# Optimization experiments

Hardware: AMD Instinct MI355X
Metric: run time of the kernel (lower is better)

The kernel has to match this reference:

```python
import jax, jax.numpy as jnp
import numpy as np

EPS = 1e-8

def _layernorm(x, gamma, beta):
    # torch-style: std with Bessel correction (ddof=1), eps added to std
    D = x.shape[-1]
    mean = jnp.mean(x, axis=-1, keepdims=True)
    var = jnp.sum((x - mean) ** 2, axis=-1, keepdims=True) / (D - 1)
    std = jnp.sqrt(var)
    return (x - mean) / (std + EPS) * gamma + beta


def setup_inputs() -> dict:
    key = jax.random.key(0)
    B, T, D, H = 1, 2048, 1024, 16
    Dh = D // H
    ks = jax.random.split(key, 8)
    s = 0.02
    return {
        "x": jax.random.normal(ks[0], (B, T, D), jnp.float32),
        "wq": jax.random.normal(ks[1], (H, D, Dh), jnp.float32) * s,
        "wk": jax.random.normal(ks[2], (H, D, Dh), jnp.float32) * s,
        "wv": jax.random.normal(ks[3], (H, D, Dh), jnp.float32) * s,
        "wo": jax.random.normal(ks[4], (D, D), jnp.float32) * s,
        "bo": jnp.zeros((D,), jnp.float32),
        "ln1_g": jnp.ones((D,), jnp.float32),
        "ln1_b": jnp.zeros((D,), jnp.float32),
        "ln2_g": jnp.ones((D,), jnp.float32),
        "ln2_b": jnp.zeros((D,), jnp.float32),
        "w1": jax.random.normal(ks[5], (D, 4 * D), jnp.float32) * s,
        "b1": jnp.zeros((4 * D,), jnp.float32),
        "w2": jax.random.normal(ks[6], (4 * D, D), jnp.float32) * s,
        "b2": jnp.zeros((D,), jnp.float32),
    }


def reference(x, wq, wk, wv, wo, bo, ln1_g, ln1_b, ln2_g, ln2_b, w1, b1, w2, b2):
    B, T, D = x.shape
    H, _, Dh = wq.shape
    # --- attention sublayer (dropout p used at eval => identity) ---
    h = _layernorm(x, ln1_g, ln1_b)
    q = jnp.einsum('btd,hde->bhte', h, wq)
    k = jnp.einsum('btd,hde->bhte', h, wk)
    v = jnp.einsum('btd,hde->bhte', h, wv)
    scores = jnp.einsum('bhte,bhse->bhts', q, k) / jnp.sqrt(jnp.float32(Dh))
    causal = jnp.triu(jnp.ones((T, T), bool), 1)  # True above diagonal => masked
    scores = jnp.where(causal, -jnp.inf, scores)
    attn = jax.nn.softmax(scores, axis=-1)
    ctx = jnp.einsum('bhts,bhse->bthe', attn, v).reshape(B, T, H * Dh)
    att_out = ctx @ wo + bo
    x = x + att_out
    # --- FFN sublayer ---
    h2 = _layernorm(x, ln2_g, ln2_b)
    ffn = jax.nn.gelu(h2 @ w1 + b1, approximate=False) @ w2 + b2
    return x + ffn
```

## Files before the change

kernel.cpp:

```cpp
#include <hip/hip_runtime.h>
#include <hip/hip_bf16.h>
#include <math.h>

typedef unsigned short bf16u;
typedef __attribute__((ext_vector_type(8))) short short8;
typedef __attribute__((ext_vector_type(4))) float floatx4;

__device__ __forceinline__ float bf2f(bf16u u) {
  union { unsigned int i; float f; } c;
  c.i = ((unsigned int)u) << 16;
  return c.f;
}
__device__ __forceinline__ bf16u f2bf(float f) {
  union { float f; unsigned int i; } c;
  c.f = f;
  unsigned int lsb = (c.i >> 16) & 1u;
  c.i += 0x7fffu + lsb;
  return (bf16u)(c.i >> 16);
}

__device__ __forceinline__ void load_lds16(const void* g, void* l) {
  __builtin_amdgcn_global_load_lds(
      (const __attribute__((address_space(1))) void*)g,
      (__attribute__((address_space(3))) void*)l, 16, 0, 0);
}

__global__ __launch_bounds__(256) void ln_kernel(
    const float* __restrict__ x, bf16u* __restrict__ out,
    const float* __restrict__ gamma, const float* __restrict__ beta) {
  const int row = blockIdx.x;
  const int tid = threadIdx.x;
  const int lane = tid & 63, wave = tid >> 6;
  __shared__ float red[4];
  const float* xr = x + (size_t)row * 1024;
  float v[4];
#pragma unroll
  for (int i = 0; i < 4; i++) v[i] = xr[tid + i * 256];
  float s = v[0] + v[1] + v[2] + v[3];
#pragma unroll
  for (int off = 32; off; off >>= 1) s += __shfl_down(s, off);
  if (lane == 0) red[wave] = s;
  __syncthreads();
  const float mean = (red[0] + red[1] + red[2] + red[3]) * (1.0f / 1024.0f);
  __syncthreads();
  float sq = 0.f;
#pragma unroll
  for (int i = 0; i < 4; i++) { float d = v[i] - mean; sq += d * d; }
#pragma unroll
  for (int off = 32; off; off >>= 1) sq += __shfl_down(sq, off);
  if (lane == 0) red[wave] = sq;
  __syncthreads();
  const float var = (red[0] + red[1] + red[2] + red[3]) * (1.0f / 1023.0f);
  const float inv = 1.0f / (sqrtf(var) + 1e-8f);
  bf16u* orow = out + (size_t)row * 1024;
#pragma unroll
  for (int i = 0; i < 4; i++) {
    int idx = tid + i * 256;
    orow[idx] = f2bf((v[i] - mean) * inv * gamma[idx] + beta[idx]);
  }
}

__global__ __launch_bounds__(256) void pack_weights(
    const float* __restrict__ wq, const float* __restrict__ wk,
    const float* __restrict__ wv, const float* __restrict__ wo,
    const float* __restrict__ w1, const float* __restrict__ w2,
    bf16u* __restrict__ WqkvT, bf16u* __restrict__ woT,
    bf16u* __restrict__ w1T, bf16u* __restrict__ w2T) {
  __shared__ bf16u tile[32][33];
  const int id = blockIdx.x;
  const float* in; bf16u* out; int R, C, bx, by;
  if (id < 3072) {
    int job = id >> 10, rem = id & 1023;
    int head = rem >> 6, t = rem & 63;
    bx = t & 1; by = t >> 1;
    in = (job == 0 ? wq : (job == 1 ? wk : wv)) + head * 65536;
    out = WqkvT + job * 1048576 + head * 65536;
    R = 1024; C = 64;
  } else if (id < 4096) {
    int rem = id - 3072; bx = rem & 31; by = rem >> 5;
    in = wo; out = woT; R = 1024; C = 1024;
  } else if (id < 8192) {
    int rem = id - 4096; bx = rem & 127; by = rem >> 7;
    in = w1; out = w1T; R = 1024; C = 4096;
  } else {
    int rem = id - 8192; bx = rem & 31; by = rem >> 5;
    in = w2; out = w2T; R = 4096; C = 1024;
  }
  const int bc = bx * 32, br = by * 32;
  const int lx = threadIdx.x & 31, ly = threadIdx.x >> 5;
#pragma unroll
  for (int i = 0; i < 32; i += 8)
    tile[ly + i][lx] = f2bf(in[(size_t)(br + ly + i) * C + bc + lx]);
  __syncthreads();
#pragma unroll
  for (int i = 0; i < 32; i += 8)
    out[(size_t)(bc + ly + i) * R + br + lx] = tile[lx][ly + i];
}

__global__ __launch_bounds__(256) void transpose_b(
    const bf16u* __restrict__ in, bf16u* __restrict__ out,
    int ins, int coff, int outs) {
  __shared__ bf16u tile[32][33];
  const int bc = blockIdx.x * 32, br = blockIdx.y * 32;
  const int lx = threadIdx.x & 31, ly = threadIdx.x >> 5;
#pragma unroll
  for (int i = 0; i < 32; i += 8)
    tile[ly + i][lx] = in[(size_t)(br + ly + i) * ins + coff + bc + lx];
  __syncthreads();
#pragma unroll
  for (int i = 0; i < 32; i += 8)
    out[(size_t)(bc + ly + i) * outs + br + lx] = tile[lx][ly + i];
}

template <int BM, int BN, int WGR, int WGC, int EPI>
__global__ __launch_bounds__(256, 4) void gemm_bt(
    const bf16u* __restrict__ A, const bf16u* __restrict__ Bt,
    const float* __restrict__ bias, const float* __restrict__ res,
    void* __restrict__ Cout, int M, int N, int K, int kchunk) {
  constexpr int BK = 64;
  constexpr int TM = BM / WGR, TN = BN / WGC;
  constexpr int NI = TM / 16, NJ = TN / 16;
  alignas(16) __shared__ bf16u sA[BM * BK];
  alignas(16) __shared__ bf16u sB[BN * BK];
  const int tid = threadIdx.x, lane = tid & 63, wave = tid >> 6;
  const int wr = wave / WGC, wc = wave % WGC;
  const int quad = lane >> 4, l16 = lane & 15;
  const int m0 = blockIdx.y * BM, n0 = blockIdx.x * BN;
  const int kz = blockIdx.z;
  const int kbeg = kz * kchunk;
  const int kend = (kbeg + kchunk < K) ? (kbeg + kchunk) : K;

  floatx4 acc[NI][NJ] = {};
  constexpr int ACH = BM * BK / 8;
  constexpr int BCH = BN * BK / 8;

  for (int k0 = kbeg; k0 < kend; k0 += BK) {
#pragma unroll
    for (int c = tid; c < ACH; c += 256) {
      int r = c >> 3, kc = ((c ^ r) & 7) * 8;
      load_lds16(A + (size_t)(m0 + r) * K + k0 + kc, (void*)(sA + c * 8));
    }
#pragma unroll
    for (int c = tid; c < BCH; c += 256) {
      int r = c >> 3, kc = ((c ^ r) & 7) * 8;
      load_lds16(Bt + (size_t)(n0 + r) * K + k0 + kc, (void*)(sB + c * 8));
    }
    __syncthreads();
#pragma unroll
    for (int kk = 0; kk < BK; kk += 32) {
      const int ch = (kk >> 3) + quad;
      short8 af[NI], bf[NJ];
#pragma unroll
      for (int i = 0; i < NI; i++) {
        const int R = wr * TM + i * 16 + l16;
        af[i] = *(const short8*)(sA + R * BK + ((ch ^ (R & 7)) << 3));
      }
#pragma unroll
      for (int j = 0; j < NJ; j++) {
        const int R = wc * TN + j * 16 + l16;
        bf[j] = *(const short8*)(sB + R * BK + ((ch ^ (R & 7)) << 3));
      }
#pragma unroll
      for (int i = 0; i < NI; i++)
#pragma unroll
        for (int j = 0; j < NJ; j++)
          acc[i][j] = __builtin_amdgcn_mfma_f32_16x16x32_bf16(af[i], bf[j], acc[i][j], 0, 0, 0);
    }
    __syncthreads();
  }

  float* pout = (float*)Cout;
  if constexpr (EPI == 3) pout += (size_t)kz * M * N;
#pragma unroll
  for (int j = 0; j < NJ; j++) {
    const int col = n0 + wc * TN + j * 16 + l16;
    float bv = 0.0f;
    if constexpr (EPI == 1 || EPI == 2) bv = bias[col];
#pragma unroll
    for (int i = 0; i < NI; i++) {
#pragma unroll
      for (int r = 0; r < 4; r++) {
        const int row = m0 + wr * TM + i * 16 + quad * 4 + r;
        const size_t o = (size_t)row * N + col;
        const float v = acc[i][j][r];
        if constexpr (EPI == 0) {
          ((bf16u*)Cout)[o] = f2bf(v);
        } else if constexpr (EPI == 1) {
          pout[o] = v + bv + res[o];
        } else if constexpr (EPI == 2) {
          float t = v + bv;
          ((bf16u*)Cout)[o] = f2bf(0.5f * t * (1.0f + erff(t * 0.70710678118654752f)));
        } else {
          pout[o] = v;
        }
      }
    }
  }
}

__global__ __launch_bounds__(256) void reduce2_kernel(
    const float* __restrict__ part, const float* __restrict__ bias,
    const float* __restrict__ res, float* __restrict__ out,
    int N, size_t total) {
  size_t i = ((size_t)blockIdx.x * 256 + threadIdx.x) * 4;
  if (i >= total) return;
  float4 a = *(const float4*)(part + i);
  float4 b = *(const float4*)(part + total + i);
  float4 r = *(const float4*)(res + i);
  float4 bv = *(const float4*)(bias + (int)(i & (size_t)(N - 1)));
  float4 o;
  o.x = a.x + b.x + r.x + bv.x;
  o.y = a.y + b.y + r.y + bv.y;
  o.z = a.z + b.z + r.z + bv.z;
  o.w = a.w + b.w + r.w + bv.w;
  *(float4*)(out + i) = o;
}

template <int NT, bool MASK>
__device__ __forceinline__ void attn_tile(
    const bf16u* sQ, const bf16u* sK, const bf16u* sVt, bf16u* sP,
    floatx4* aco, floatx4& acc_l, short8 ones,
    int q0, int c0, int wave, int quad, int l16) {
  const int rq = wave * 16 + l16;
  floatx4 s[NT] = {};
#pragma unroll
  for (int kk = 0; kk < 64; kk += 32) {
    const int ch = (kk >> 3) + quad;
    short8 aq = *(const short8*)(sQ + rq * 64 + ((ch ^ (rq & 7)) << 3));
#pragma unroll
    for (int nt = 0; nt < NT; nt++) {
      const int rk = nt * 16 + l16;
      short8 bk = *(const short8*)(sK + rk * 64 + ((ch ^ (rk & 7)) << 3));
      s[nt] = __builtin_amdgcn_mfma_f32_16x16x32_bf16(bk, aq, s[nt], 0, 0, 0);
    }
  }
  const float C = 0.125f * 1.44269504088896f;
  const int qrow = q0 + rq;
#pragma unroll
  for (int nt = 0; nt < NT; nt++)
#pragma unroll
    for (int r = 0; r < 4; r++) {
      float t = s[nt][r] * C;
      if constexpr (MASK) {
        const int kpos = c0 + nt * 16 + quad * 4 + r;
        if (kpos > qrow) t = -__builtin_inff();
      }
      s[nt][r] = __builtin_amdgcn_exp2f(t);
    }
  __syncthreads();
#pragma unroll
  for (int nt = 0; nt < NT; nt++) {
    unsigned int lo = (unsigned int)f2bf(s[nt][0]) | ((unsigned int)f2bf(s[nt][1]) << 16);
    unsigned int hi = (unsigned int)f2bf(s[nt][2]) | ((unsigned int)f2bf(s[nt][3]) << 16);
    uint2 pk; pk.x = lo; pk.y = hi;
    const int e0 = nt * 16 + quad * 4;
    const int cch = e0 >> 3, sub = e0 & 7;
    *(uint2*)(sP + rq * 128 + ((cch ^ (rq & 7)) << 3) + sub) = pk;
  }
  __syncthreads();
#pragma unroll
  for (int kk = 0; kk < NT * 16; kk += 32) {
    const int ch = (kk >> 3) + quad;
    short8 ap = *(const short8*)(sP + rq * 128 + ((ch ^ (rq & 7)) << 3));
#pragma unroll
    for (int dt = 0; dt < 4; dt++) {
      const int rv = dt * 16 + l16;
      short8 bv = *(const short8*)(sVt + rv * 128 + ((ch ^ (rv & 7)) << 3));
      aco[dt] = __builtin_amdgcn_mfma_f32_16x16x32_bf16(ap, bv, aco[dt], 0, 0, 0);
    }
    acc_l = __builtin_amdgcn_mfma_f32_16x16x32_bf16(ap, ones, acc_l, 0, 0, 0);
  }
}

template <int NZ>
__global__ __launch_bounds__(256, 4) void flash_attn(
    const bf16u* __restrict__ QKV, const bf16u* __restrict__ Vt,
    bf16u* __restrict__ partO, float* __restrict__ partL) {
  const int qb = 31 - blockIdx.x;
  const int h = blockIdx.y;
  const int z = blockIdx.z;
  const int tid = threadIdx.x, lane = tid & 63, wave = tid >> 6;
  const int quad = lane >> 4, l16 = lane & 15;
  alignas(16) __shared__ bf16u sQ[64 * 64];
  alignas(16) __shared__ bf16u sK[128 * 64];
  alignas(16) __shared__ bf16u sVt[64 * 128];
  bf16u* sP = sK;
  const int q0 = qb * 64;

  for (int c = tid; c < 512; c += 256) {
    int r = c >> 3, cc = c & 7;
    *(uint4*)(sQ + r * 64 + ((cc ^ (r & 7)) << 3)) =
        *(const uint4*)(QKV + (size_t)(q0 + r) * 3072 + h * 64 + cc * 8);
  }

  floatx4 acc_l = {0.f, 0.f, 0.f, 0.f};
  floatx4 aco[4] = {};
  short8 ones;
#pragma unroll
  for (int u = 0; u < 8; u++) ones[u] = (short)0x3F80;

  const int nkt = (qb >> 1) + 1;
  for (int kt = z; kt < nkt; kt += NZ) {
    const int c0 = kt * 128;
    __syncthreads();
    for (int c = tid; c < 1024; c += 256) {
      int r = c >> 3, cc = c & 7;
      *(uint4*)(sK + r * 64 + ((cc ^ (r & 7)) << 3)) =
          *(const uint4*)(QKV + (size_t)(c0 + r) * 3072 + 1024 + h * 64 + cc * 8);
    }
    for (int c = tid; c < 1024; c += 256) {
      int e = c >> 4, cc = c & 15;
      *(uint4*)(sVt + e * 128 + ((cc ^ (e & 7)) << 3)) =
          *(const uint4*)(Vt + (size_t)(h * 64 + e) * 2048 + c0 + cc * 8);
    }
    __syncthreads();
    if (kt == nkt - 1) {
      if ((qb & 1) == 0)
        attn_tile<4, true>(sQ, sK, sVt, sP, aco, acc_l, ones, q0, c0, wave, quad, l16);
      else
        attn_tile<8, true>(sQ, sK, sVt, sP, aco, acc_l, ones, q0, c0, wave, quad, l16);
    } else {
      attn_tile<8, false>(sQ, sK, sVt, sP, aco, acc_l, ones, q0, c0, wave, quad, l16);
    }
  }
  bf16u* po = partO + ((size_t)z * 2048 + q0) * 1024 + h * 64;
#pragma unroll
  for (int dt = 0; dt < 4; dt++)
#pragma unroll
    for (int r = 0; r < 4; r++)
      po[(wave * 16 + quad * 4 + r) * 1024 + dt * 16 + l16] = f2bf(aco[dt][r]);
  if (l16 == 0) {
#pragma unroll
    for (int r = 0; r < 4; r++)
      partL[((size_t)z * 2048 + q0 + wave * 16 + quad * 4 + r) * 16 + h] = acc_l[r];
  }
}

template <int NZ>
__global__ __launch_bounds__(256) void attn_reduce(
    const bf16u* __restrict__ partO, const float* __restrict__ partL,
    bf16u* __restrict__ ctx) {
  const int t = blockIdx.x;
  const int col = threadIdx.x * 4;
  const int h = col >> 6;
  float l = 0.f;
#pragma unroll
  for (int z = 0; z < NZ; z++) l += partL[((size_t)z * 2048 + t) * 16 + h];
  float o0 = 0.f, o1 = 0.f, o2 = 0.f, o3 = 0.f;
#pragma unroll
  for (int z = 0; z < NZ; z++) {
    uint2 v = *(const uint2*)(partO + ((size_t)z * 2048 + t) * 1024 + col);
    o0 += bf2f((bf16u)(v.x & 0xffff)); o1 += bf2f((bf16u)(v.x >> 16));
    o2 += bf2f((bf16u)(v.y & 0xffff)); o3 += bf2f((bf16u)(v.y >> 16));
  }
  const float inv = 1.0f / l;
  uint2 pk;
  pk.x = (unsigned int)f2bf(o0 * inv) | ((unsigned int)f2bf(o1 * inv) << 16);
  pk.y = (unsigned int)f2bf(o2 * inv) | ((unsigned int)f2bf(o3 * inv) << 16);
  *(uint2*)(ctx + (size_t)t * 1024 + col) = pk;
}

extern "C" void kernel_launch(void* const* d_in, const int* in_sizes, int n_in,
                              void* d_out, int out_size, void* d_ws, size_t ws_size,
                              hipStream_t stream) {
  (void)in_sizes; (void)n_in; (void)out_size; (void)ws_size;
  const float* x   = (const float*)d_in[0];
  const float* wq  = (const float*)d_in[1];
  const float* wk  = (const float*)d_in[2];
  const float* wv  = (const float*)d_in[3];
  const float* wo  = (const float*)d_in[4];
  const float* bo  = (const float*)d_in[5];
  const float* g1  = (const float*)d_in[6];
  const float* be1 = (const float*)d_in[7];
  const float* g2  = (const float*)d_in[8];
  const float* be2 = (const float*)d_in[9];
  const float* w1  = (const float*)d_in[10];
  const float* bb1 = (const float*)d_in[11];
  const float* w2  = (const float*)d_in[12];
  const float* bb2 = (const float*)d_in[13];

  char* p = (char*)d_ws;
  const size_t MB = 1024 * 1024;
  constexpr int NZ = 4;
  bf16u* WqkvT = (bf16u*)(p + 0 * MB);
  bf16u* woT   = (bf16u*)(p + 6 * MB);
  bf16u* w1T   = (bf16u*)(p + 8 * MB);
  bf16u* w2T   = (bf16u*)(p + 16 * MB);
  bf16u* multi = (bf16u*)(p + 24 * MB);
  bf16u* QKV   = (bf16u*)(p + 28 * MB);
  float* partL = (float*)(p + 40 * MB);
  bf16u* partO = (bf16u*)(p + 41 * MB);
  bf16u* mid   = (bf16u*)(p + 28 * MB);
  float* x1    = (float*)(p + 49 * MB);
  float* partF = (float*)(p + 0 * MB);
  bf16u* hln = multi, *Vtr = multi, *ctx = multi, *h2 = multi;

  pack_weights<<<12288, 256, 0, stream>>>(wq, wk, wv, wo, w1, w2,
                                          WqkvT, woT, w1T, w2T);

  ln_kernel<<<2048, 256, 0, stream>>>(x, hln, g1, be1);
  gemm_bt<64, 128, 2, 2, 0><<<dim3(24, 32, 1), 256, 0, stream>>>(
      hln, WqkvT, nullptr, nullptr, QKV, 2048, 3072, 1024, 1024);
  transpose_b<<<dim3(32, 64), 256, 0, stream>>>(QKV, Vtr, 3072, 2048, 2048);
  flash_attn<NZ><<<dim3(32, 16, NZ), 256, 0, stream>>>(QKV, Vtr, partO, partL);
  attn_reduce<NZ><<<2048, 256, 0, stream>>>(partO, partL, ctx);
  gemm_bt<32, 64, 2, 2, 1><<<dim3(16, 64, 1), 256, 0, stream>>>(
      ctx, woT, bo, x, x1, 2048, 1024, 1024, 1024);
  ln_kernel<<<2048, 256, 0, stream>>>(x1, h2, g2, be2);
  gemm_bt<64, 128, 2, 2, 2><<<dim3(32, 32, 1), 256, 0, stream>>>(
      h2, w1T, bb1, nullptr, mid, 2048, 4096, 1024, 1024);
  gemm_bt<64, 64, 2, 2, 3><<<dim3(16, 32, 2), 256, 0, stream>>>(
      mid, w2T, nullptr, nullptr, partF, 2048, 1024, 4096, 2048);
  reduce2_kernel<<<2048, 256, 0, stream>>>(partF, bb2, x1, (float*)d_out,
                                           1024, (size_t)2048 * 1024);
}
```

Baseline: 281.1 us.

## Shrink attention KV tile and prefetch next K/V via async LDS loads

Reduces the flash-attention KV tile from 128 to 64 keys with separate P buffer, so masking is only on the diagonal tile and LDS per block shrinks. K and V for the next iteration are loaded with global_load_lds directly into LDS, K issued after the P write and V after the second barrier, overlapping loads with PV MFMAs. Launch bounds raised to 5 blocks per CU to increase occupancy, at risk of register pressure and more loop iterations/barriers per block.

Result: faster. 268.0 us (-4.7%).

```diff
diff --git a/kernel.cpp b/kernel.cpp
--- a/kernel.cpp
+++ b/kernel.cpp
@@ -216,64 +216,8 @@
   *(float4*)(out + i) = o;
 }
 
-template <int NT, bool MASK>
-__device__ __forceinline__ void attn_tile(
-    const bf16u* sQ, const bf16u* sK, const bf16u* sVt, bf16u* sP,
-    floatx4* aco, floatx4& acc_l, short8 ones,
-    int q0, int c0, int wave, int quad, int l16) {
-  const int rq = wave * 16 + l16;
-  floatx4 s[NT] = {};
-#pragma unroll
-  for (int kk = 0; kk < 64; kk += 32) {
-    const int ch = (kk >> 3) + quad;
-    short8 aq = *(const short8*)(sQ + rq * 64 + ((ch ^ (rq & 7)) << 3));
-#pragma unroll
-    for (int nt = 0; nt < NT; nt++) {
-      const int rk = nt * 16 + l16;
-      short8 bk = *(const short8*)(sK + rk * 64 + ((ch ^ (rk & 7)) << 3));
-      s[nt] = __builtin_amdgcn_mfma_f32_16x16x32_bf16(bk, aq, s[nt], 0, 0, 0);
-    }
-  }
-  const float C = 0.125f * 1.44269504088896f;
-  const int qrow = q0 + rq;
-#pragma unroll
-  for (int nt = 0; nt < NT; nt++)
-#pragma unroll
-    for (int r = 0; r < 4; r++) {
-      float t = s[nt][r] * C;
-      if constexpr (MASK) {
-        const int kpos = c0 + nt * 16 + quad * 4 + r;
-        if (kpos > qrow) t = -__builtin_inff();
-      }
-      s[nt][r] = __builtin_amdgcn_exp2f(t);
-    }
-  __syncthreads();
-#pragma unroll
-  for (int nt = 0; nt < NT; nt++) {
-    unsigned int lo = (unsigned int)f2bf(s[nt][0]) | ((unsigned int)f2bf(s[nt][1]) << 16);
-    unsigned int hi = (unsigned int)f2bf(s[nt][2]) | ((unsigned int)f2bf(s[nt][3]) << 16);
-    uint2 pk; pk.x = lo; pk.y = hi;
-    const int e0 = nt * 16 + quad * 4;
-    const int cch = e0 >> 3, sub = e0 & 7;
-    *(uint2*)(sP + rq * 128 + ((cch ^ (rq & 7)) << 3) + sub) = pk;
-  }
-  __syncthreads();
-#pragma unroll
-  for (int kk = 0; kk < NT * 16; kk += 32) {
-    const int ch = (kk >> 3) + quad;
-    short8 ap = *(const short8*)(sP + rq * 128 + ((ch ^ (rq & 7)) << 3));
-#pragma unroll
-    for (int dt = 0; dt < 4; dt++) {
-      const int rv = dt * 16 + l16;
-      short8 bv = *(const short8*)(sVt + rv * 128 + ((ch ^ (rv & 7)) << 3));
-      aco[dt] = __builtin_amdgcn_mfma_f32_16x16x32_bf16(ap, bv, aco[dt], 0, 0, 0);
-    }
-    acc_l = __builtin_amdgcn_mfma_f32_16x16x32_bf16(ap, ones, acc_l, 0, 0, 0);
-  }
-}
-
 template <int NZ>
-__global__ __launch_bounds__(256, 4) void flash_attn(
+__global__ __launch_bounds__(256, 5) void flash_attn(
     const bf16u* __restrict__ QKV, const bf16u* __restrict__ Vt,
     bf16u* __restrict__ partO, float* __restrict__ partL) {
   const int qb = 31 - blockIdx.x;
@@ -282,16 +226,33 @@
   const int tid = threadIdx.x, lane = tid & 63, wave = tid >> 6;
   const int quad = lane >> 4, l16 = lane & 15;
   alignas(16) __shared__ bf16u sQ[64 * 64];
-  alignas(16) __shared__ bf16u sK[128 * 64];
-  alignas(16) __shared__ bf16u sVt[64 * 128];
-  bf16u* sP = sK;
+  alignas(16) __shared__ bf16u sK[64 * 64];
+  alignas(16) __shared__ bf16u sVt[64 * 64];
+  alignas(16) __shared__ bf16u sP[64 * 64];
   const int q0 = qb * 64;
-
+  const int nkt = qb + 1;
+  const int rq = wave * 16 + l16;
+
+#pragma unroll
   for (int c = tid; c < 512; c += 256) {
-    int r = c >> 3, cc = c & 7;
-    *(uint4*)(sQ + r * 64 + ((cc ^ (r & 7)) << 3)) =
-        *(const uint4*)(QKV + (size_t)(q0 + r) * 3072 + h * 64 + cc * 8);
-  }
+    int r = c >> 3, kc = (c ^ r) & 7;
+    load_lds16(QKV + (size_t)(q0 + r) * 3072 + h * 64 + kc * 8, (void*)(sQ + c * 8));
+  }
+  int kt = z;
+  if (kt < nkt) {
+    const int c0 = kt * 64;
+#pragma unroll
+    for (int c = tid; c < 512; c += 256) {
+      int r = c >> 3, kc = (c ^ r) & 7;
+      load_lds16(QKV + (size_t)(c0 + r) * 3072 + 1024 + h * 64 + kc * 8, (void*)(sK + c * 8));
+    }
+#pragma unroll
+    for (int c = tid; c < 512; c += 256) {
+      int e = c >> 3, kc = (c ^ e) & 7;
+      load_lds16(Vt + (size_t)(h * 64 + e) * 2048 + c0 + kc * 8, (void*)(sVt + c * 8));
+    }
+  }
+  __syncthreads();
 
   floatx4 acc_l = {0.f, 0.f, 0.f, 0.f};
   floatx4 aco[4] = {};
@@ -299,30 +260,76 @@
 #pragma unroll
   for (int u = 0; u < 8; u++) ones[u] = (short)0x3F80;
 
-  const int nkt = (qb >> 1) + 1;
-  for (int kt = z; kt < nkt; kt += NZ) {
-    const int c0 = kt * 128;
+  for (; kt < nkt; kt += NZ) {
+    const int c0 = kt * 64;
+    floatx4 s[4] = {};
+#pragma unroll
+    for (int kk = 0; kk < 64; kk += 32) {
+      const int ch = (kk >> 3) + quad;
+      short8 aq = *(const short8*)(sQ + rq * 64 + ((ch ^ (rq & 7)) << 3));
+#pragma unroll
+      for (int nt = 0; nt < 4; nt++) {
+        const int rk = nt * 16 + l16;
+        short8 bk = *(const short8*)(sK + rk * 64 + ((ch ^ (rk & 7)) << 3));
+        s[nt] = __builtin_amdgcn_mfma_f32_16x16x32_bf16(bk, aq, s[nt], 0, 0, 0);
+      }
+    }
+    const float C = 0.125f * 1.44269504088896f;
+    const bool diag = (kt == qb);
+#pragma unroll
+    for (int nt = 0; nt < 4; nt++)
+#pragma unroll
+      for (int r = 0; r < 4; r++) {
+        float t = s[nt][r] * C;
+        if (diag) {
+          const int kpos = c0 + nt * 16 + quad * 4 + r;
+          if (kpos > q0 + rq) t = -__builtin_inff();
+        }
+        s[nt][r] = __builtin_amdgcn_exp2f(t);
+      }
+#pragma unroll
+    for (int nt = 0; nt < 4; nt++) {
+      unsigned int lo = (unsigned int)f2bf(s[nt][0]) | ((unsigned int)f2bf(s[nt][1]) << 16);
+      unsigned int hi = (unsigned int)f2bf(s[nt][2]) | ((unsigned int)f2bf(s[nt][3]) << 16);
+      uint2 pk; pk.x = lo; pk.y = hi;
+      const int e0 = nt * 16 + quad * 4;
+      const int cch = e0 >> 3, sub = e0 & 7;
+      *(uint2*)(sP + rq * 64 + ((cch ^ (rq & 7)) << 3) + sub) = pk;
+    }
     __syncthreads();
-    for (int c = tid; c < 1024; c += 256) {
-      int r = c >> 3, cc = c & 7;
-      *(uint4*)(sK + r * 64 + ((cc ^ (r & 7)) << 3)) =
-          *(const uint4*)(QKV + (size_t)(c0 + r) * 3072 + 1024 + h * 64 + cc * 8);
-    }
-    for (int c = tid; c < 1024; c += 256) {
-      int e = c >> 4, cc = c & 15;
-      *(uint4*)(sVt + e * 128 + ((cc ^ (e & 7)) << 3)) =
-          *(const uint4*)(Vt + (size_t)(h * 64 + e) * 2048 + c0 + cc * 8);
+    if (kt + NZ < nkt) {
+      const int c0n = (kt + NZ) * 64;
+#pragma unroll
+      for (int c = tid; c < 512; c += 256) {
+        int r = c >> 3, kc = (c ^ r) & 7;
+        load_lds16(QKV + (size_t)(c0n + r) * 3072 + 1024 + h * 64 + kc * 8,
+                   (void*)(sK + c * 8));
+      }
+    }
+#pragma unroll
+    for (int kk = 0; kk < 64; kk += 32) {
+      const int ch = (kk >> 3) + quad;
+      short8 ap = *(const short8*)(sP + rq * 64 + ((ch ^ (rq & 7)) << 3));
+#pragma unroll
+      for (int dt = 0; dt < 4; dt++) {
+        const int rv = dt * 16 + l16;
+        short8 bv = *(const short8*)(sVt + rv * 64 + ((ch ^ (rv & 7)) << 3));
+        aco[dt] = __builtin_amdgcn_mfma_f32_16x16x32_bf16(ap, bv, aco[dt], 0, 0, 0);
+      }
+      acc_l = __builtin_amdgcn_mfma_f32_16x16x32_bf16(ap, ones, acc_l, 0, 0, 0);
     }
     __syncthreads();
-    if (kt == nkt - 1) {
-      if ((qb & 1) == 0)
-        attn_tile<4, true>(sQ, sK, sVt, sP, aco, acc_l, ones, q0, c0, wave, quad, l16);
-      else
-        attn_tile<8, true>(sQ, sK, sVt, sP, aco, acc_l, ones, q0, c0, wave, quad, l16);
-    } else {
-      attn_tile<8, false>(sQ, sK, sVt, sP, aco, acc_l, ones, q0, c0, wave, quad, l16);
-    }
-  }
+    if (kt + NZ < nkt) {
+      const int c0n = (kt + NZ) * 64;
+#pragma unroll
+      for (int c = tid; c < 512; c += 256) {
+        int e = c >> 3, kc = (c ^ e) & 7;
+        load_lds16(Vt + (size_t)(h * 64 + e) * 2048 + c0n + kc * 8,
+                   (void*)(sVt + c * 8));
+      }
+    }
+  }
+
   bf16u* po = partO + ((size_t)z * 2048 + q0) * 1024 + h * 64;
 #pragma unroll
   for (int dt = 0; dt < 4; dt++)
```
